# Performance work log

Measured on AMD Instinct MI355X. Metric: run time of the kernel, lower is better.

Reference implementation:

```python
import jax, jax.numpy as jnp
import numpy as np

B, T, E = 4, 2048, 1024
NUM_HEADS = 16
HEAD_SIZE = E // NUM_HEADS


def _rope_tables(T, E):
    # thetas over pairs, repeat_interleave by 2 -> shape (E,)
    thetas = 10000.0 ** (-jnp.arange(0, E, 2, dtype=jnp.float32) / E)
    thetas = jnp.repeat(thetas, 2)
    angles = jnp.arange(T, dtype=jnp.float32)[:, None] * thetas[None, :]  # (T, E)
    return jnp.sin(angles), jnp.cos(angles)


def _rotate(x, sin, cos):
    # x: (B, T, E); pairs (x0, x1) -> (-x1, x0)
    Bx, Tx, Ex = x.shape
    xp = x.reshape(Bx, Tx, Ex // 2, 2)
    rot = jnp.stack([-xp[..., 1], xp[..., 0]], axis=-1).reshape(Bx, Tx, Ex)
    return x * cos + rot * sin


def setup_inputs() -> dict:
    key = jax.random.key(0)
    ks = jax.random.split(key, 6)
    scale = 1.0 / np.sqrt(E)
    return {
        "input": jax.random.normal(ks[0], (B, T, E), dtype=jnp.float32),
        "Wq": jax.random.normal(ks[1], (E, E), dtype=jnp.float32) * scale,
        "Wk": jax.random.normal(ks[2], (E, E), dtype=jnp.float32) * scale,
        "Wv": jax.random.normal(ks[3], (E, E), dtype=jnp.float32) * scale,
        "Wo": jax.random.normal(ks[4], (E, E), dtype=jnp.float32) * scale,
        "bo": jnp.zeros((E,), dtype=jnp.float32),
    }


def reference(input, Wq, Wk, Wv, Wo, bo):
    Bx, Tx, Ex = input.shape
    sin, cos = _rope_tables(Tx, Ex)
    rx = _rotate(input, sin, cos)
    q = rx @ Wq.T
    k = rx @ Wk.T
    v = input @ Wv.T
    # (B, H, T, hd)
    def split_heads(t):
        return t.reshape(Bx, Tx, NUM_HEADS, HEAD_SIZE).transpose(0, 2, 1, 3)
    q, k, v = split_heads(q), split_heads(k), split_heads(v)
    scores = jnp.einsum("bhqd,bhkd->bhqk", q, k)
    causal = jnp.tril(jnp.ones((Tx, Tx), dtype=bool))
    scores = jnp.where(causal[None, None], scores, -jnp.inf) / np.sqrt(HEAD_SIZE)
    attn = jax.nn.softmax(scores, axis=-1)  # dropout omitted (eval mode)
    out = jnp.einsum("bhqk,bhkd->bhqd", attn, v)
    out = out.transpose(0, 2, 1, 3).reshape(Bx, Tx, Ex)
    return out @ Wo.T + bo
```

## Files before the change

### kernel.cpp

```cpp
#include <hip/hip_runtime.h>

typedef unsigned short u16;
typedef unsigned int   u32;
typedef __attribute__((ext_vector_type(4))) float f32x4;
typedef __attribute__((ext_vector_type(8))) __bf16 bf16x8;
typedef __attribute__((ext_vector_type(2))) u32  u32x2;
typedef __attribute__((ext_vector_type(4))) u32  u32x4;

#define LDS_CAST(p) ((__attribute__((address_space(3))) void*)(p))
#define GLB_CAST(p) ((const __attribute__((address_space(1))) void*)(p))

__device__ __forceinline__ void load_lds16(const void* g, void* l) {
    __builtin_amdgcn_global_load_lds(GLB_CAST(g), LDS_CAST(l), 16, 0, 0);
}

__device__ __forceinline__ u32 lds_off(const void* p) {
    return (u32)(size_t)(const __attribute__((address_space(3))) void*)p;
}

__device__ __forceinline__ u16 f2bf(float f) {
    union { float f; u32 u; } v; v.f = f;
    u32 r = (v.u + 0x7FFFu + ((v.u >> 16) & 1u)) >> 16;
    return (u16)r;
}

__device__ __forceinline__ u16 bfc(float f) {
    return __builtin_bit_cast(u16, (__bf16)f);
}

__device__ __forceinline__ float exp2fast(float x) {
#if __has_builtin(__builtin_amdgcn_exp2f)
    return __builtin_amdgcn_exp2f(x);
#else
    return __expf(x * 0.6931471805599453f);
#endif
}

__global__ __launch_bounds__(256) void rope_cast(const float* __restrict__ x,
                                                 u16* __restrict__ xb,
                                                 u16* __restrict__ rxb) {
    int idx = blockIdx.x * 256 + threadIdx.x;
    int e2 = (idx & 511) * 2;
    int t  = (idx >> 9) & 2047;
    float2 v = *(const float2*)&x[(size_t)idx * 2];
    float theta = expf(-0.0089944730194981f * (float)e2);
    float angle = (float)t * theta;
    float sa, ca;
    sincosf(angle, &sa, &ca);
    float r0 = v.x * ca - v.y * sa;
    float r1 = v.y * ca + v.x * sa;
    u32 xp  = (u32)f2bf(v.x) | ((u32)f2bf(v.y) << 16);
    u32 rxp = (u32)f2bf(r0)  | ((u32)f2bf(r1)  << 16);
    *(u32*)&xb[(size_t)idx * 2]  = xp;
    *(u32*)&rxb[(size_t)idx * 2] = rxp;
}

__global__ __launch_bounds__(256) void wcast(const float* __restrict__ a,
                                             const float* __restrict__ b,
                                             const float* __restrict__ c,
                                             const float* __restrict__ d,
                                             u16* __restrict__ out) {
    int i = blockIdx.x * 256 + threadIdx.x;
    int w = i >> 20, j = i & 1048575;
    float v = (w == 0) ? a[j] : (w == 1) ? b[j] : (w == 2) ? c[j] : d[j];
    out[i] = f2bf(v);
}

template <int MODE>
__global__ __launch_bounds__(256) void gemm128(const u16* __restrict__ A0,
                                               const u16* __restrict__ A1,
                                               const u16* __restrict__ W,
                                               u16* __restrict__ outb,
                                               float* __restrict__ outf,
                                               const float* __restrict__ bias) {
    constexpr int Kd = 1024;
    __shared__ u16 As[128 * 64];
    __shared__ u16 Bs[128 * 64];
    const int tid = threadIdx.x;
    const int m0 = blockIdx.x * 128;
    const int n0 = blockIdx.y * 128;
    const u16* A = (MODE == 0 && n0 >= 2048) ? A1 : A0;
    const int wid = tid >> 6, lane = tid & 63;
    const int wr = wid >> 1, wc = wid & 1;
    const int lr = lane & 15, lhi = lane >> 4;

    f32x4 acc[4][4] = {};

    for (int k0 = 0; k0 < Kd; k0 += 64) {
        if (k0) __syncthreads();
#pragma unroll
        for (int i = 0; i < 4; ++i) {
            int cidx = tid + 256 * i;
            int row = cidx >> 3, col = (cidx & 7) * 8;
            load_lds16(A + (size_t)(m0 + row) * Kd + k0 + col, &As[row * 64 + col]);
        }
#pragma unroll
        for (int i = 0; i < 4; ++i) {
            int cidx = tid + 256 * i;
            int row = cidx >> 3, col = (cidx & 7) * 8;
            load_lds16(W + (size_t)(n0 + row) * Kd + k0 + col, &Bs[row * 64 + col]);
        }
        __syncthreads();
#pragma unroll
        for (int c = 0; c < 2; ++c) {
            bf16x8 a[4], b[4];
#pragma unroll
            for (int m = 0; m < 4; ++m)
                a[m] = *(const bf16x8*)&As[(wr * 64 + m * 16 + lr) * 64 + c * 32 + lhi * 8];
#pragma unroll
            for (int n = 0; n < 4; ++n)
                b[n] = *(const bf16x8*)&Bs[(wc * 64 + n * 16 + lr) * 64 + c * 32 + lhi * 8];
#pragma unroll
            for (int m = 0; m < 4; ++m)
#pragma unroll
                for (int n = 0; n < 4; ++n)
                    acc[m][n] = __builtin_amdgcn_mfma_f32_16x16x32_bf16(a[m], b[n], acc[m][n], 0, 0, 0);
        }
    }

#pragma unroll
    for (int m = 0; m < 4; ++m) {
        int rowb = m0 + wr * 64 + m * 16 + lhi * 4;
#pragma unroll
        for (int n = 0; n < 4; ++n) {
            int col = n0 + wc * 64 + n * 16 + lr;
#pragma unroll
            for (int r = 0; r < 4; ++r) {
                int mg = rowb + r;
                float v = acc[m][n][r];
                if (MODE == 0) {
                    int bb = mg >> 11, t = mg & 2047;
                    int hg = col >> 6, d = col & 63;
                    outb[(size_t)(hg >> 4) * 8388608 +
                         (((size_t)(bb * 16 + (hg & 15)) * 2048) + t) * 64 + d] = bfc(v);
                } else {
                    outf[(size_t)mg * 1024 + col] = v + bias[col];
                }
            }
        }
    }
}

__device__ __forceinline__ void attn_pass(const bf16x8 (&qa)[2], f32x4 (&acc)[4],
                                          float (&m_i)[4], float (&l_i)[4],
                                          const u16* ks, const u16* vcur, u32 vsb,
                                          u16* pw, int lr, int lhi,
                                          int kv0, int q0w, bool diag, bool use_tr) {
    f32x4 s4[4] = {};
    __builtin_amdgcn_s_setprio(1);
#pragma unroll
    for (int c = 0; c < 2; ++c)
#pragma unroll
        for (int n = 0; n < 4; ++n) {
            int r = n * 16 + lr;
            bf16x8 kb = *(const bf16x8*)&ks[r * 64 + ((c * 32 + lhi * 8) ^ ((r & 7) * 8))];
            s4[n] = __builtin_amdgcn_mfma_f32_16x16x32_bf16(qa[c], kb, s4[n], 0, 0, 0);
        }
    __builtin_amdgcn_s_setprio(0);

    if (diag) {
#pragma unroll
        for (int n = 0; n < 4; ++n) {
            int kvg = kv0 + n * 16 + lr;
#pragma unroll
            for (int r = 0; r < 4; ++r)
                if (kvg > q0w + lhi * 4 + r) s4[n][r] = -1e30f;
        }
    }

    float mx[4] = { -1e30f, -1e30f, -1e30f, -1e30f };
#pragma unroll
    for (int n = 0; n < 4; ++n)
#pragma unroll
        for (int r = 0; r < 4; ++r) mx[r] = fmaxf(mx[r], s4[n][r]);
#pragma unroll
    for (int off = 8; off; off >>= 1)
#pragma unroll
        for (int r = 0; r < 4; ++r) mx[r] = fmaxf(mx[r], __shfl_xor(mx[r], off));

    bool up = false;
#pragma unroll
    for (int r = 0; r < 4; ++r) up = up || (mx[r] > m_i[r] + 8.0f);
    if (__any((int)up)) {
#pragma unroll
        for (int r = 0; r < 4; ++r) {
            float mnew = fmaxf(m_i[r], mx[r]);
            float sc = exp2fast(m_i[r] - mnew);
            m_i[r] = mnew;
            l_i[r] *= sc;
#pragma unroll
            for (int nd = 0; nd < 4; ++nd) acc[nd][r] *= sc;
        }
    }

    float rs[4] = { 0.f, 0.f, 0.f, 0.f };
#pragma unroll
    for (int n = 0; n < 4; ++n)
#pragma unroll
        for (int r = 0; r < 4; ++r) {
            float pv = exp2fast(s4[n][r] - m_i[r]);
            rs[r] += pv;
            int qloc = lhi * 4 + r;
            pw[qloc * 64 + ((n * 16 + lr) ^ ((qloc & 7) * 8))] = bfc(pv);
        }
#pragma unroll
    for (int off = 8; off; off >>= 1)
#pragma unroll
        for (int r = 0; r < 4; ++r) rs[r] += __shfl_xor(rs[r], off);
#pragma unroll
    for (int r = 0; r < 4; ++r) l_i[r] += rs[r];

    __builtin_amdgcn_s_setprio(1);
#pragma unroll
    for (int c = 0; c < 2; ++c) {
        bf16x8 pa = *(const bf16x8*)&pw[lr * 64 + ((c * 32 + lhi * 8) ^ ((lr & 7) * 8))];
        union { bf16x8 v; u32 w[4]; u16 h[8]; } vb[4];
        if (use_tr) {
            u32x2 lo[4], hi[4];
#pragma unroll
            for (int nd = 0; nd < 4; ++nd) {
                u32 a = vsb + (u32)((c * 32 + lhi * 8 + nd) * 128 + lr * 2);
                asm volatile("ds_read_b64_tr_b16 %0, %2\n\t"
                             "ds_read_b64_tr_b16 %1, %2 offset:512"
                             : "=&v"(lo[nd]), "=&v"(hi[nd]) : "v"(a));
            }
            asm volatile("s_waitcnt lgkmcnt(0)" ::: "memory");
            __builtin_amdgcn_sched_barrier(0);
#pragma unroll
            for (int nd = 0; nd < 4; ++nd) {
                vb[nd].w[0] = lo[nd].x; vb[nd].w[1] = lo[nd].y;
                vb[nd].w[2] = hi[nd].x; vb[nd].w[3] = hi[nd].y;
            }
        } else {
#pragma unroll
            for (int nd = 0; nd < 4; ++nd)
#pragma unroll
                for (int i = 0; i < 8; ++i) {
                    int k = c * 32 + lhi * 8 + i;
                    vb[nd].h[i] = vcur[((k >> 2) << 8) + (nd << 6) + ((k & 3) << 4) + lr];
                }
        }
#pragma unroll
        for (int nd = 0; nd < 4; ++nd)
            acc[nd] = __builtin_amdgcn_mfma_f32_16x16x32_bf16(pa, vb[nd].v, acc[nd], 0, 0, 0);
    }
    __builtin_amdgcn_s_setprio(0);
}

__global__ __launch_bounds__(256) void attn64(const u16* __restrict__ Q,
                                              const u16* __restrict__ K,
                                              const u16* __restrict__ V,
                                              u16* __restrict__ O) {
    constexpr int T = 2048;
    __shared__ u16 Ks[2][64 * 64];
    __shared__ u16 Vs[2][64 * 64];
    __shared__ u16 Ps[4][16 * 64];
    const int tid = threadIdx.x, wid = tid >> 6, lane = tid & 63;
    const int lr = lane & 15, lhi = lane >> 4;
    const int bh = blockIdx.y;
    const int qtA = blockIdx.x;
    const int qtB = 31 - qtA;
    const int q0wA = qtA * 64 + wid * 16;
    const int q0wB = qtB * 64 + wid * 16;
    const size_t base = (size_t)bh * T * 64;
    const u16* Qp = Q + base;
    const u16* Kp = K + base;
    const u16* Vp = V + base;

    const float QS = 0.18033688011112042f;
    bf16x8 qaA[2], qaB[2];
#pragma unroll
    for (int c = 0; c < 2; ++c) {
        bf16x8 tA = *(const bf16x8*)&Qp[(size_t)(q0wA + lr) * 64 + c * 32 + lhi * 8];
        bf16x8 tB = *(const bf16x8*)&Qp[(size_t)(q0wB + lr) * 64 + c * 32 + lhi * 8];
        bf16x8 oA, oB;
#pragma unroll
        for (int i = 0; i < 8; ++i) {
            oA[i] = (__bf16)((float)tA[i] * QS);
            oB[i] = (__bf16)((float)tB[i] * QS);
        }
        qaA[c] = oA; qaB[c] = oB;
    }

    f32x4 accA[4] = {}, accB[4] = {};
    float m_iA[4], l_iA[4], m_iB[4], l_iB[4];
#pragma unroll
    for (int r = 0; r < 4; ++r) {
        m_iA[r] = -1e30f; l_iA[r] = 0.f;
        m_iB[r] = -1e30f; l_iB[r] = 0.f;
    }

    {
        u16* vt = (u16*)&Vs[0][0];
#pragma unroll
        for (int j = 0; j < 16; ++j) vt[tid * 16 + j] = (u16)(tid * 16 + j);
    }
    __syncthreads();
    bool use_tr;
    {
        const u32 vsb0 = lds_off(&Vs[0][0]);
        bool ok = true;
#pragma unroll
        for (int t = 0; t < 2; ++t) {
            const int c = t ? 1 : 0, nd = t ? 3 : 0;
            u32 a = vsb0 + (u32)((c * 32 + lhi * 8 + nd) * 128 + lr * 2);
            u32x2 lo, hi;
            asm volatile("ds_read_b64_tr_b16 %0, %2\n\t"
                         "ds_read_b64_tr_b16 %1, %2 offset:512"
                         : "=&v"(lo), "=&v"(hi) : "v"(a));
            asm volatile("s_waitcnt lgkmcnt(0)" ::: "memory");
            __builtin_amdgcn_sched_barrier(0);
            union { u32 w[4]; u16 h[8]; } u;
            u.w[0] = lo.x; u.w[1] = lo.y; u.w[2] = hi.x; u.w[3] = hi.y;
#pragma unroll
            for (int i = 0; i < 8; ++i) {
                int k = c * 32 + lhi * 8 + i;
                int e = ((k >> 2) << 8) + (nd << 6) + ((k & 3) << 4) + lr;
                ok = ok && (u.h[i] == (u16)e);
            }
        }
        use_tr = (bool)__all((int)ok);
    }
    __syncthreads();

#define STAGE(bb, kv0s)                                                          \
    {                                                                            \
        _Pragma("unroll")                                                        \
        for (int i = 0; i < 2; ++i) {                                            \
            int q = tid + 256 * i;                                               \
            int krow = q >> 3;                                                   \
            int kcol = ((q & 7) ^ (krow & 7)) * 8;                               \
            load_lds16(Kp + (size_t)((kv0s) + krow) * 64 + kcol, &Ks[bb][q * 8]);\
            int vk = ((q >> 5) << 2) + ((q >> 1) & 3);                           \
            int vd = (((q >> 3) & 3) << 4) + ((q & 1) << 3);                     \
            load_lds16(Vp + (size_t)((kv0s) + vk) * 64 + vd, &Vs[bb][q * 8]);    \
        }                                                                        \
    }

    STAGE(0, 0);
    __syncthreads();

    u16* pw = Ps[wid];
    int buf = 0;
    for (int kt = 0; kt <= qtB; ++kt) {
        const int kv0 = kt * 64;
        if (kt < qtB) STAGE(buf ^ 1, kv0 + 64);

        const u16* ks = Ks[buf];
        const u16* vcur = Vs[buf];
        const u32 vsb = lds_off(vcur);

        if (kt <= qtA)
            attn_pass(qaA, accA, m_iA, l_iA, ks, vcur, vsb, pw, lr, lhi,
                      kv0, q0wA, kt == qtA, use_tr);
        attn_pass(qaB, accB, m_iB, l_iB, ks, vcur, vsb, pw, lr, lhi,
                  kv0, q0wB, kt == qtB, use_tr);

        __syncthreads();
        buf ^= 1;
    }
#undef STAGE

    const int b = bh >> 4, h = bh & 15;
#pragma unroll
    for (int nd = 0; nd < 4; ++nd)
#pragma unroll
        for (int r = 0; r < 4; ++r) {
            int d = h * 64 + nd * 16 + lr;
            int qgA = q0wA + lhi * 4 + r;
            int qgB = q0wB + lhi * 4 + r;
            O[(size_t)(b * 2048 + qgA) * 1024 + d] = bfc(accA[nd][r] / l_iA[r]);
            O[(size_t)(b * 2048 + qgB) * 1024 + d] = bfc(accB[nd][r] / l_iB[r]);
        }
}

extern "C" void kernel_launch(void* const* d_in, const int* in_sizes, int n_in,
                              void* d_out, int out_size, void* d_ws, size_t ws_size,
                              hipStream_t stream) {
    const float* x  = (const float*)d_in[0];
    const float* Wq = (const float*)d_in[1];
    const float* Wk = (const float*)d_in[2];
    const float* Wv = (const float*)d_in[3];
    const float* Wo = (const float*)d_in[4];
    const float* bo = (const float*)d_in[5];

    char* ws = (char*)d_ws;
    u16* Wqb = (u16*)ws;
    u16* Wob = Wqb + 3 * (1 << 20);
    u16* xb  = (u16*)(ws + (size_t)8 * 1024 * 1024);
    u16* rxb = xb  + (size_t)8388608;
    u16* Qb  = rxb + (size_t)8388608;
    u16* Kb  = Qb  + (size_t)8388608;
    u16* Vb  = Kb  + (size_t)8388608;
    u16* Ob  = Vb  + (size_t)8388608;

    rope_cast<<<16384, 256, 0, stream>>>(x, xb, rxb);
    wcast<<<16384, 256, 0, stream>>>(Wq, Wk, Wv, Wo, Wqb);

    gemm128<0><<<dim3(64, 24), 256, 0, stream>>>(rxb, xb, Wqb, Qb, nullptr, nullptr);

    attn64<<<dim3(16, 64), 256, 0, stream>>>(Qb, Kb, Vb, Ob);

    gemm128<1><<<dim3(64, 8), 256, 0, stream>>>(Ob, Ob, Wob, nullptr, (float*)d_out, bo);
}
```

Before: 363.8 us.

## Enlarge attention query tile to 128 rows per block for more K/V reuse

The attention kernel now gives each block two 128-row query tiles (paired front/back for causal balance) instead of two 64-row tiles, and each wave handles two 16-row fragments per tile. Every staged K/V tile is read from LDS once and reused across both fragments, which halves the number of K/V loads per query row. In exchange, register pressure rises because four accumulator sets are live, only 512 blocks are launched instead of 1024, and the diagonal masking is handled per fragment.

Result: slower. 433.2 us (+19.1%).

```diff
diff --git a/kernel.cpp b/kernel.cpp
--- a/kernel.cpp
+++ b/kernel.cpp
@@ -141,12 +141,17 @@
     }
 }
 
-__device__ __forceinline__ void attn_pass(const bf16x8 (&qa)[2], f32x4 (&acc)[4],
-                                          float (&m_i)[4], float (&l_i)[4],
-                                          const u16* ks, const u16* vcur, u32 vsb,
-                                          u16* pw, int lr, int lhi,
-                                          int kv0, int q0w, bool diag, bool use_tr) {
-    f32x4 s4[4] = {};
+__device__ __forceinline__ void attn_pass2(const bf16x8 (&qa)[2][2],
+                                           f32x4 (&acc)[2][4],
+                                           float (&m_i)[2][4], float (&l_i)[2][4],
+                                           const u16* ks, const u16* vcur, u32 vsb,
+                                           u16* pw0, u16* pw1,
+                                           int lr, int lhi, int kv0,
+                                           int R0, int R1, bool use_tr) {
+    const bool act[2] = { kv0 <= R0 + 15, kv0 <= R1 + 15 };
+    const int  Rf[2]  = { R0, R1 };
+
+    f32x4 s[2][4] = {};
     __builtin_amdgcn_s_setprio(1);
 #pragma unroll
     for (int c = 0; c < 2; ++c)
@@ -154,141 +159,167 @@
         for (int n = 0; n < 4; ++n) {
             int r = n * 16 + lr;
             bf16x8 kb = *(const bf16x8*)&ks[r * 64 + ((c * 32 + lhi * 8) ^ ((r & 7) * 8))];
-            s4[n] = __builtin_amdgcn_mfma_f32_16x16x32_bf16(qa[c], kb, s4[n], 0, 0, 0);
+            if (act[0]) s[0][n] = __builtin_amdgcn_mfma_f32_16x16x32_bf16(qa[0][c], kb, s[0][n], 0, 0, 0);
+            if (act[1]) s[1][n] = __builtin_amdgcn_mfma_f32_16x16x32_bf16(qa[1][c], kb, s[1][n], 0, 0, 0);
         }
     __builtin_amdgcn_s_setprio(0);
 
-    if (diag) {
-#pragma unroll
-        for (int n = 0; n < 4; ++n) {
-            int kvg = kv0 + n * 16 + lr;
-#pragma unroll
-            for (int r = 0; r < 4; ++r)
-                if (kvg > q0w + lhi * 4 + r) s4[n][r] = -1e30f;
-        }
-    }
-
-    float mx[4] = { -1e30f, -1e30f, -1e30f, -1e30f };
-#pragma unroll
-    for (int n = 0; n < 4; ++n)
-#pragma unroll
-        for (int r = 0; r < 4; ++r) mx[r] = fmaxf(mx[r], s4[n][r]);
-#pragma unroll
-    for (int off = 8; off; off >>= 1)
-#pragma unroll
-        for (int r = 0; r < 4; ++r) mx[r] = fmaxf(mx[r], __shfl_xor(mx[r], off));
-
-    bool up = false;
-#pragma unroll
-    for (int r = 0; r < 4; ++r) up = up || (mx[r] > m_i[r] + 8.0f);
-    if (__any((int)up)) {
-#pragma unroll
-        for (int r = 0; r < 4; ++r) {
-            float mnew = fmaxf(m_i[r], mx[r]);
-            float sc = exp2fast(m_i[r] - mnew);
-            m_i[r] = mnew;
-            l_i[r] *= sc;
-#pragma unroll
-            for (int nd = 0; nd < 4; ++nd) acc[nd][r] *= sc;
-        }
-    }
-
-    float rs[4] = { 0.f, 0.f, 0.f, 0.f };
-#pragma unroll
-    for (int n = 0; n < 4; ++n)
-#pragma unroll
-        for (int r = 0; r < 4; ++r) {
-            float pv = exp2fast(s4[n][r] - m_i[r]);
-            rs[r] += pv;
-            int qloc = lhi * 4 + r;
-            pw[qloc * 64 + ((n * 16 + lr) ^ ((qloc & 7) * 8))] = bfc(pv);
-        }
-#pragma unroll
-    for (int off = 8; off; off >>= 1)
-#pragma unroll
-        for (int r = 0; r < 4; ++r) rs[r] += __shfl_xor(rs[r], off);
-#pragma unroll
-    for (int r = 0; r < 4; ++r) l_i[r] += rs[r];
-
-    __builtin_amdgcn_s_setprio(1);
-#pragma unroll
-    for (int c = 0; c < 2; ++c) {
-        bf16x8 pa = *(const bf16x8*)&pw[lr * 64 + ((c * 32 + lhi * 8) ^ ((lr & 7) * 8))];
-        union { bf16x8 v; u32 w[4]; u16 h[8]; } vb[4];
-        if (use_tr) {
-            u32x2 lo[4], hi[4];
+#pragma unroll
+    for (int f = 0; f < 2; ++f) {
+        if (!act[f]) continue;
+        if (kv0 + 63 > Rf[f]) {
+#pragma unroll
+            for (int n = 0; n < 4; ++n) {
+                int kvg = kv0 + n * 16 + lr;
+#pragma unroll
+                for (int r = 0; r < 4; ++r)
+                    if (kvg > Rf[f] + lhi * 4 + r) s[f][n][r] = -1e30f;
+            }
+        }
+        float mx[4] = { -1e30f, -1e30f, -1e30f, -1e30f };
+#pragma unroll
+        for (int n = 0; n < 4; ++n)
+#pragma unroll
+            for (int r = 0; r < 4; ++r) mx[r] = fmaxf(mx[r], s[f][n][r]);
+#pragma unroll
+        for (int off = 8; off; off >>= 1)
+#pragma unroll
+            for (int r = 0; r < 4; ++r) mx[r] = fmaxf(mx[r], __shfl_xor(mx[r], off));
+
+        bool up = false;
+#pragma unroll
+        for (int r = 0; r < 4; ++r) up = up || (mx[r] > m_i[f][r] + 8.0f);
+        if (__any((int)up)) {
+#pragma unroll
+            for (int r = 0; r < 4; ++r) {
+                float mnew = fmaxf(m_i[f][r], mx[r]);
+                float sc = exp2fast(m_i[f][r] - mnew);
+                m_i[f][r] = mnew;
+                l_i[f][r] *= sc;
+#pragma unroll
+                for (int nd = 0; nd < 4; ++nd) acc[f][nd][r] *= sc;
+            }
+        }
+        u16* pwf = f ? pw1 : pw0;
+        float rs[4] = { 0.f, 0.f, 0.f, 0.f };
+#pragma unroll
+        for (int n = 0; n < 4; ++n)
+#pragma unroll
+            for (int r = 0; r < 4; ++r) {
+                float pv = exp2fast(s[f][n][r] - m_i[f][r]);
+                rs[r] += pv;
+                int qloc = lhi * 4 + r;
+                pwf[qloc * 64 + ((n * 16 + lr) ^ ((qloc & 7) * 8))] = bfc(pv);
+            }
+#pragma unroll
+        for (int off = 8; off; off >>= 1)
+#pragma unroll
+            for (int r = 0; r < 4; ++r) rs[r] += __shfl_xor(rs[r], off);
+#pragma unroll
+        for (int r = 0; r < 4; ++r) l_i[f][r] += rs[r];
+    }
+
+    union VB { bf16x8 v; u32 w[4]; u16 h[8]; };
+    VB vb[2][4];
+    bf16x8 pa[2][2];
+#pragma unroll
+    for (int f = 0; f < 2; ++f) {
+        if (!act[f]) continue;
+        const u16* pwf = f ? pw1 : pw0;
+#pragma unroll
+        for (int c = 0; c < 2; ++c)
+            pa[f][c] = *(const bf16x8*)&pwf[lr * 64 + ((c * 32 + lhi * 8) ^ ((lr & 7) * 8))];
+    }
+    if (use_tr) {
+        u32x2 lo[2][4], hi[2][4];
+#pragma unroll
+        for (int c = 0; c < 2; ++c)
 #pragma unroll
             for (int nd = 0; nd < 4; ++nd) {
                 u32 a = vsb + (u32)((c * 32 + lhi * 8 + nd) * 128 + lr * 2);
                 asm volatile("ds_read_b64_tr_b16 %0, %2\n\t"
                              "ds_read_b64_tr_b16 %1, %2 offset:512"
-                             : "=&v"(lo[nd]), "=&v"(hi[nd]) : "v"(a));
-            }
-            asm volatile("s_waitcnt lgkmcnt(0)" ::: "memory");
-            __builtin_amdgcn_sched_barrier(0);
+                             : "=&v"(lo[c][nd]), "=&v"(hi[c][nd]) : "v"(a));
+            }
+        asm volatile("s_waitcnt lgkmcnt(0)" ::: "memory");
+        __builtin_amdgcn_sched_barrier(0);
+#pragma unroll
+        for (int c = 0; c < 2; ++c)
 #pragma unroll
             for (int nd = 0; nd < 4; ++nd) {
-                vb[nd].w[0] = lo[nd].x; vb[nd].w[1] = lo[nd].y;
-                vb[nd].w[2] = hi[nd].x; vb[nd].w[3] = hi[nd].y;
-            }
-        } else {
+                vb[c][nd].w[0] = lo[c][nd].x; vb[c][nd].w[1] = lo[c][nd].y;
+                vb[c][nd].w[2] = hi[c][nd].x; vb[c][nd].w[3] = hi[c][nd].y;
+            }
+    } else {
+#pragma unroll
+        for (int c = 0; c < 2; ++c)
 #pragma unroll
             for (int nd = 0; nd < 4; ++nd)
 #pragma unroll
                 for (int i = 0; i < 8; ++i) {
                     int k = c * 32 + lhi * 8 + i;
-                    vb[nd].h[i] = vcur[((k >> 2) << 8) + (nd << 6) + ((k & 3) << 4) + lr];
+                    vb[c][nd].h[i] = vcur[((k >> 2) << 8) + (nd << 6) + ((k & 3) << 4) + lr];
                 }
-        }
-#pragma unroll
-        for (int nd = 0; nd < 4; ++nd)
-            acc[nd] = __builtin_amdgcn_mfma_f32_16x16x32_bf16(pa, vb[nd].v, acc[nd], 0, 0, 0);
+    }
+    __builtin_amdgcn_s_setprio(1);
+#pragma unroll
+    for (int f = 0; f < 2; ++f) {
+        if (!act[f]) continue;
+#pragma unroll
+        for (int c = 0; c < 2; ++c)
+#pragma unroll
+            for (int nd = 0; nd < 4; ++nd)
+                acc[f][nd] = __builtin_amdgcn_mfma_f32_16x16x32_bf16(pa[f][c], vb[c][nd].v, acc[f][nd], 0, 0, 0);
     }
     __builtin_amdgcn_s_setprio(0);
 }
 
-__global__ __launch_bounds__(256) void attn64(const u16* __restrict__ Q,
-                                              const u16* __restrict__ K,
-                                              const u16* __restrict__ V,
-                                              u16* __restrict__ O) {
+__global__ __launch_bounds__(256) void attn128(const u16* __restrict__ Q,
+                                               const u16* __restrict__ K,
+                                               const u16* __restrict__ V,
+                                               u16* __restrict__ O) {
     constexpr int T = 2048;
     __shared__ u16 Ks[2][64 * 64];
     __shared__ u16 Vs[2][64 * 64];
-    __shared__ u16 Ps[4][16 * 64];
+    __shared__ u16 Ps[4][2][16 * 64];
     const int tid = threadIdx.x, wid = tid >> 6, lane = tid & 63;
     const int lr = lane & 15, lhi = lane >> 4;
     const int bh = blockIdx.y;
-    const int qtA = blockIdx.x;
-    const int qtB = 31 - qtA;
-    const int q0wA = qtA * 64 + wid * 16;
-    const int q0wB = qtB * 64 + wid * 16;
+    const int qt[2] = { (int)blockIdx.x, 15 - (int)blockIdx.x };
     const size_t base = (size_t)bh * T * 64;
     const u16* Qp = Q + base;
     const u16* Kp = K + base;
     const u16* Vp = V + base;
 
+    int R[2][2];
+#pragma unroll
+    for (int p = 0; p < 2; ++p)
+#pragma unroll
+        for (int f = 0; f < 2; ++f) R[p][f] = qt[p] * 128 + f * 64 + wid * 16;
+
     const float QS = 0.18033688011112042f;
-    bf16x8 qaA[2], qaB[2];
-#pragma unroll
-    for (int c = 0; c < 2; ++c) {
-        bf16x8 tA = *(const bf16x8*)&Qp[(size_t)(q0wA + lr) * 64 + c * 32 + lhi * 8];
-        bf16x8 tB = *(const bf16x8*)&Qp[(size_t)(q0wB + lr) * 64 + c * 32 + lhi * 8];
-        bf16x8 oA, oB;
-#pragma unroll
-        for (int i = 0; i < 8; ++i) {
-            oA[i] = (__bf16)((float)tA[i] * QS);
-            oB[i] = (__bf16)((float)tB[i] * QS);
-        }
-        qaA[c] = oA; qaB[c] = oB;
-    }
-
-    f32x4 accA[4] = {}, accB[4] = {};
-    float m_iA[4], l_iA[4], m_iB[4], l_iB[4];
-#pragma unroll
-    for (int r = 0; r < 4; ++r) {
-        m_iA[r] = -1e30f; l_iA[r] = 0.f;
-        m_iB[r] = -1e30f; l_iB[r] = 0.f;
-    }
+    bf16x8 qa[2][2][2];
+#pragma unroll
+    for (int p = 0; p < 2; ++p)
+#pragma unroll
+        for (int f = 0; f < 2; ++f)
+#pragma unroll
+            for (int c = 0; c < 2; ++c) {
+                bf16x8 t = *(const bf16x8*)&Qp[(size_t)(R[p][f] + lr) * 64 + c * 32 + lhi * 8];
+                bf16x8 o;
+#pragma unroll
+                for (int i = 0; i < 8; ++i) o[i] = (__bf16)((float)t[i] * QS);
+                qa[p][f][c] = o;
+            }
+
+    f32x4 acc[2][2][4] = {};
+    float m_i[2][2][4], l_i[2][2][4];
+#pragma unroll
+    for (int p = 0; p < 2; ++p)
+#pragma unroll
+        for (int f = 0; f < 2; ++f)
+#pragma unroll
+            for (int r = 0; r < 4; ++r) { m_i[p][f][r] = -1e30f; l_i[p][f][r] = 0.f; }
 
     {
         u16* vt = (u16*)&Vs[0][0];
@@ -340,21 +371,22 @@
     STAGE(0, 0);
     __syncthreads();
 
-    u16* pw = Ps[wid];
+    const int ntA = 2 * qt[0] + 2;
+    const int ntB = 2 * qt[1] + 2;
     int buf = 0;
-    for (int kt = 0; kt <= qtB; ++kt) {
+    for (int kt = 0; kt < ntB; ++kt) {
         const int kv0 = kt * 64;
-        if (kt < qtB) STAGE(buf ^ 1, kv0 + 64);
+        if (kt + 1 < ntB) STAGE(buf ^ 1, kv0 + 64);
 
         const u16* ks = Ks[buf];
         const u16* vcur = Vs[buf];
         const u32 vsb = lds_off(vcur);
 
-        if (kt <= qtA)
-            attn_pass(qaA, accA, m_iA, l_iA, ks, vcur, vsb, pw, lr, lhi,
-                      kv0, q0wA, kt == qtA, use_tr);
-        attn_pass(qaB, accB, m_iB, l_iB, ks, vcur, vsb, pw, lr, lhi,
-                  kv0, q0wB, kt == qtB, use_tr);
+        if (kt < ntA)
+            attn_pass2(qa[0], acc[0], m_i[0], l_i[0], ks, vcur, vsb,
+                       Ps[wid][0], Ps[wid][1], lr, lhi, kv0, R[0][0], R[0][1], use_tr);
+        attn_pass2(qa[1], acc[1], m_i[1], l_i[1], ks, vcur, vsb,
+                   Ps[wid][0], Ps[wid][1], lr, lhi, kv0, R[1][0], R[1][1], use_tr);
 
         __syncthreads();
         buf ^= 1;
@@ -363,15 +395,17 @@
 
     const int b = bh >> 4, h = bh & 15;
 #pragma unroll
-    for (int nd = 0; nd < 4; ++nd)
-#pragma unroll
-        for (int r = 0; r < 4; ++r) {
-            int d = h * 64 + nd * 16 + lr;
-            int qgA = q0wA + lhi * 4 + r;
-            int qgB = q0wB + lhi * 4 + r;
-            O[(size_t)(b * 2048 + qgA) * 1024 + d] = bfc(accA[nd][r] / l_iA[r]);
-            O[(size_t)(b * 2048 + qgB) * 1024 + d] = bfc(accB[nd][r] / l_iB[r]);
-        }
+    for (int p = 0; p < 2; ++p)
+#pragma unroll
+        for (int f = 0; f < 2; ++f)
+#pragma unroll
+            for (int nd = 0; nd < 4; ++nd)
+#pragma unroll
+                for (int r = 0; r < 4; ++r) {
+                    int d = h * 64 + nd * 16 + lr;
+                    int qg = R[p][f] + lhi * 4 + r;
+                    O[(size_t)(b * 2048 + qg) * 1024 + d] = bfc(acc[p][f][nd][r] / l_i[p][f][r]);
+                }
 }
 
 extern "C" void kernel_launch(void* const* d_in, const int* in_sizes, int n_in,
@@ -399,7 +433,7 @@
 
     gemm128<0><<<dim3(64, 24), 256, 0, stream>>>(rxb, xb, Wqb, Qb, nullptr, nullptr);
 
-    attn64<<<dim3(16, 64), 256, 0, stream>>>(Qb, Kb, Vb, Ob);
+    attn128<<<dim3(8, 64), 256, 0, stream>>>(Qb, Kb, Vb, Ob);
 
     gemm128<1><<<dim3(64, 8), 256, 0, stream>>>(Ob, Ob, Wob, nullptr, (float*)d_out, bo);
 }
```
